# Performance work log

Hardware: AMD Instinct MI355X
Metric: run time of the kernel (lower is better)

Reference implementation:

```python
import jax, jax.numpy as jnp
import numpy as np

N_NODES = 100000
N_EDGES = 1600000
D = 128


def setup_inputs() -> dict:
    key = jax.random.key(0)
    ks = jax.random.split(key, 8)
    x = jax.random.normal(ks[0], (N_NODES, D), dtype=jnp.float32)
    edge_index = jax.random.randint(ks[1], (2, N_EDGES), 0, N_NODES, dtype=jnp.int64)
    # Linear weights ~ fan-in scaled init
    scale = 1.0 / np.sqrt(D)
    W1 = jax.random.normal(ks[2], (D, D), dtype=jnp.float32) * scale
    W2 = jax.random.normal(ks[3], (D, D), dtype=jnp.float32) * scale
    W3 = jax.random.normal(ks[4], (D, D), dtype=jnp.float32) * scale
    b1 = jnp.zeros((D,), jnp.float32)
    b2 = jnp.zeros((D,), jnp.float32)
    b3 = jnp.zeros((D,), jnp.float32)
    # train_eps=True, PyG initializes eps to 0
    eps1 = jnp.zeros((), jnp.float32)
    eps2 = jnp.zeros((), jnp.float32)
    eps3 = jnp.zeros((), jnp.float32)
    return {"x": x, "edge_index": edge_index,
            "W1": W1, "b1": b1, "eps1": eps1,
            "W2": W2, "b2": b2, "eps2": eps2,
            "W3": W3, "b3": b3, "eps3": eps3}


def _gin_conv(x, src, dst, eps, W, b):
    # scatter-add neighbor aggregation: sum_{j in N(i)} x_j
    agg = jax.ops.segment_sum(x[src], dst, num_segments=N_NODES)  # [N, D]
    h = (1.0 + eps) * x + agg
    return jax.nn.relu(h @ W + b)


def reference(x, edge_index, W1, b1, eps1, W2, b2, eps2, W3, b3, eps3):
    src, dst = edge_index[0], edge_index[1]
    h = _gin_conv(x, src, dst, eps1, W1, b1)   # conv1 (dropout p=0 -> identity)
    h = _gin_conv(h, src, dst, eps2, W2, b2)
    h = _gin_conv(h, src, dst, eps3, W3, b3)
    return jax.nn.log_softmax(h, axis=1)
```

## Files before the change

### kernel.cpp

```cpp
#include <hip/hip_runtime.h>
#include <hip/hip_bf16.h>

#define N_NODES 100000
#define N_EDGES 1600000
#define D 128
#define NRANGE 8
#define RANGE_SZ 12500
#define SB_PER_RANGE 196
#define NBUCKET (NRANGE * SB_PER_RANGE)
#define G_PART 512
#define CH_PART 3125
#define G_DEG 128
#define CH_DEG 784

typedef __attribute__((ext_vector_type(8))) short bf16x8;
typedef __attribute__((ext_vector_type(8))) unsigned short u16x8;
typedef __attribute__((ext_vector_type(4))) float f32x4;
typedef unsigned int u32;

__device__ inline ushort f2b(float x) {
    union { float f; unsigned u; } v; v.f = x;
    unsigned r = (v.u + 0x7fff + ((v.u >> 16) & 1)) >> 16;
    return (ushort)r;
}
__device__ inline float b2f(ushort b) {
    union { unsigned u; float f; } v; v.u = ((unsigned)b) << 16;
    return v.f;
}

__global__ void x2b_kernel(const float* __restrict__ x, ushort* __restrict__ xb) {
    int i = blockIdx.x * blockDim.x + threadIdx.x;
    if (i >= N_NODES * D / 4) return;
    float4 v = ((const float4*)x)[i];
    ushort4 o;
    o.x = f2b(v.x); o.y = f2b(v.y); o.z = f2b(v.z); o.w = f2b(v.w);
    ((ushort4*)xb)[i] = o;
}


__global__ void hist1_kernel(const int* __restrict__ dst, int* __restrict__ bhist1) {
    __shared__ int lh[NRANGE];
    if (threadIdx.x < NRANGE) lh[threadIdx.x] = 0;
    __syncthreads();
    int s0 = blockIdx.x * CH_PART, s1 = s0 + CH_PART;
    if (s1 > N_EDGES) s1 = N_EDGES;
    for (int i = s0 + threadIdx.x; i < s1; i += 256)
        atomicAdd(&lh[dst[i] / RANGE_SZ], 1);
    __syncthreads();
    if (threadIdx.x < NRANGE) bhist1[blockIdx.x * NRANGE + threadIdx.x] = lh[threadIdx.x];
}

__global__ void scan1_kernel(const int* __restrict__ bhist1, int* __restrict__ cbase1,
                             int* __restrict__ rs) {
    int r = threadIdx.x >> 6, lane = threadIdx.x & 63;
    __shared__ int rtot[NRANGE], roff[NRANGE];
    int excl[8];
    int run = 0;
    #pragma unroll
    for (int seg = 0; seg < 8; ++seg) {
        int b = seg * 64 + lane;
        int v = bhist1[b * NRANGE + r];
        int sc = v;
        #pragma unroll
        for (int off = 1; off < 64; off <<= 1) {
            int y = __shfl_up(sc, off);
            if (lane >= off) sc += y;
        }
        excl[seg] = run + sc - v;
        run += __shfl(sc, 63);
    }
    if (lane == 63) rtot[r] = run;
    __syncthreads();
    if (threadIdx.x == 0) {
        int a = 0;
        for (int i = 0; i < NRANGE; ++i) { roff[i] = a; a += rtot[i]; }
    }
    __syncthreads();
    int base = roff[r];
    #pragma unroll
    for (int seg = 0; seg < 8; ++seg)
        cbase1[(seg * 64 + lane) * NRANGE + r] = base + excl[seg];
    if (threadIdx.x < NRANGE) rs[threadIdx.x] = roff[threadIdx.x];
    if (threadIdx.x == 0) rs[NRANGE] = N_EDGES;
}

__global__ void place1_kernel(const int* __restrict__ src, const int* __restrict__ dst,
                              const int* __restrict__ cbase1, u32* __restrict__ epack1) {
    __shared__ int cur[NRANGE];
    if (threadIdx.x < NRANGE) cur[threadIdx.x] = cbase1[blockIdx.x * NRANGE + threadIdx.x];
    __syncthreads();
    int s0 = blockIdx.x * CH_PART, s1 = s0 + CH_PART;
    if (s1 > N_EDGES) s1 = N_EDGES;
    for (int i = s0 + threadIdx.x; i < s1; i += 256) {
        int d = dst[i], s = src[i];
        int r = d / RANGE_SZ;
        int dl = d - r * RANGE_SZ;
        int p = atomicAdd(&cur[r], 1);
        epack1[p] = ((u32)dl << 17) | (u32)s;
    }
}

__global__ void hist2_kernel(const u32* __restrict__ epack1, const int* __restrict__ rs,
                             int* __restrict__ bhist2) {
    __shared__ int lh[SB_PER_RANGE];
    for (int i = threadIdx.x; i < SB_PER_RANGE; i += 256) lh[i] = 0;
    __syncthreads();
    int r = blockIdx.x >> 6, j = blockIdx.x & 63;
    int e0 = rs[r], e1 = rs[r + 1];
    int cs = (e1 - e0 + 63) >> 6;
    int s0 = e0 + j * cs, s1 = s0 + cs;
    if (s1 > e1) s1 = e1;
    for (int i = s0 + threadIdx.x; i < s1; i += 256)
        atomicAdd(&lh[epack1[i] >> 23], 1);
    __syncthreads();
    for (int i = threadIdx.x; i < SB_PER_RANGE; i += 256)
        bhist2[blockIdx.x * SB_PER_RANGE + i] = lh[i];
}

__global__ void scan2_kernel(const int* __restrict__ bhist2, const int* __restrict__ rs,
                             int* __restrict__ cbase2, int* __restrict__ bucket_start) {
    int r = blockIdx.x;
    __shared__ int tot[SB_PER_RANGE];
    __shared__ int base[SB_PER_RANGE];
    int sb = threadIdx.x;
    if (sb < SB_PER_RANGE) {
        int s = 0;
        for (int j = 0; j < 64; ++j) s += bhist2[(r * 64 + j) * SB_PER_RANGE + sb];
        tot[sb] = s;
    }
    __syncthreads();
    if (threadIdx.x == 0) {
        int a = 0;
        for (int i = 0; i < SB_PER_RANGE; ++i) { base[i] = a; a += tot[i]; }
    }
    __syncthreads();
    if (sb < SB_PER_RANGE) {
        int run = rs[r] + base[sb];
        bucket_start[r * SB_PER_RANGE + sb] = run;
        for (int j = 0; j < 64; ++j) {
            cbase2[(r * 64 + j) * SB_PER_RANGE + sb] = run;
            run += bhist2[(r * 64 + j) * SB_PER_RANGE + sb];
        }
    }
    if (r == NRANGE - 1 && threadIdx.x == 0) bucket_start[NBUCKET] = N_EDGES;
}

__global__ void place2_kernel(const u32* __restrict__ epack1, const int* __restrict__ rs,
                              const int* __restrict__ cbase2, u32* __restrict__ epack2) {
    __shared__ int cur[SB_PER_RANGE];
    for (int i = threadIdx.x; i < SB_PER_RANGE; i += 256)
        cur[i] = cbase2[blockIdx.x * SB_PER_RANGE + i];
    __syncthreads();
    int r = blockIdx.x >> 6, j = blockIdx.x & 63;
    int e0 = rs[r], e1 = rs[r + 1];
    int cs = (e1 - e0 + 63) >> 6;
    int s0 = e0 + j * cs, s1 = s0 + cs;
    if (s1 > e1) s1 = e1;
    for (int i = s0 + threadIdx.x; i < s1; i += 256) {
        u32 e = epack1[i];
        int sb = e >> 23;
        int p = atomicAdd(&cur[sb], 1);
        epack2[p] = e & 0x7FFFFFu;
    }
}

__global__ void sort3_kernel(const u32* __restrict__ epack2, const int* __restrict__ bucket_start,
                             int* __restrict__ row_ptr, int* __restrict__ col,
                             int* __restrict__ deg) {
    int b = blockIdx.x;
    int r = b / SB_PER_RANGE, sb = b - r * SB_PER_RANGE;
    int node_base = r * RANGE_SZ + sb * 64;
    int nb = r * RANGE_SZ + RANGE_SZ - node_base;
    if (nb > 64) nb = 64;
    int e0 = bucket_start[b], e1 = bucket_start[b + 1];
    __shared__ int hist[64], cur[64];
    if (threadIdx.x < 64) hist[threadIdx.x] = 0;
    __syncthreads();
    for (int i = e0 + threadIdx.x; i < e1; i += 256)
        atomicAdd(&hist[(epack2[i] >> 17) & 63], 1);
    __syncthreads();
    if (threadIdx.x < 64) {
        int v = hist[threadIdx.x];
        int sc = v;
        #pragma unroll
        for (int off = 1; off < 64; off <<= 1) {
            int y = __shfl_up(sc, off);
            if (threadIdx.x >= off) sc += y;
        }
        int ex = e0 + sc - v;
        cur[threadIdx.x] = ex;
        if (threadIdx.x < nb) {
            row_ptr[node_base + threadIdx.x] = ex;
            deg[node_base + threadIdx.x] = v;
        }
    }
    __syncthreads();
    for (int i = e0 + threadIdx.x; i < e1; i += 256) {
        u32 e = epack2[i];
        int l = (e >> 17) & 63;
        int p = atomicAdd(&cur[l], 1);
        col[p] = (int)(e & 0x1FFFFu);
    }
    if (b == NBUCKET - 1 && threadIdx.x == 0) row_ptr[N_NODES] = N_EDGES;
}


__global__ void deghist_kernel(const int* __restrict__ deg, int* __restrict__ bdh) {
    __shared__ int lh[128];
    if (threadIdx.x < 128) lh[threadIdx.x] = 0;
    __syncthreads();
    int s0 = blockIdx.x * CH_DEG, s1 = s0 + CH_DEG;
    if (s1 > N_NODES) s1 = N_NODES;
    for (int i = s0 + threadIdx.x; i < s1; i += 256)
        atomicAdd(&lh[min(deg[i], 127)], 1);
    __syncthreads();
    if (threadIdx.x < 128) bdh[blockIdx.x * 128 + threadIdx.x] = lh[threadIdx.x];
}

__global__ void degscan_kernel(const int* __restrict__ bdh, int* __restrict__ cbdeg) {
    __shared__ int sh[128];
    int t = threadIdx.x;
    int tot = 0;
    for (int j = 0; j < G_DEG; ++j) tot += bdh[j * 128 + t];
    sh[t] = tot;
    __syncthreads();
    if (t == 0) {
        int run = 0;
        for (int b = 127; b >= 0; --b) { int c = sh[b]; sh[b] = run; run += c; }
    }
    __syncthreads();
    int run = sh[t];
    for (int j = 0; j < G_DEG; ++j) {
        cbdeg[j * 128 + t] = run;
        run += bdh[j * 128 + t];
    }
}

__global__ void degplace_kernel(const int* __restrict__ deg, const int* __restrict__ cbdeg,
                                int* __restrict__ perm) {
    __shared__ int cur[128];
    if (threadIdx.x < 128) cur[threadIdx.x] = cbdeg[blockIdx.x * 128 + threadIdx.x];
    __syncthreads();
    int s0 = blockIdx.x * CH_DEG, s1 = s0 + CH_DEG;
    if (s1 > N_NODES) s1 = N_NODES;
    for (int i = s0 + threadIdx.x; i < s1; i += 256) {
        int p = atomicAdd(&cur[min(deg[i], 127)], 1);
        perm[p] = i;
    }
}


__global__ void aggregate_kernel(const ushort* __restrict__ xb, const int* __restrict__ row_ptr,
                                 const int* __restrict__ col, const int* __restrict__ perm,
                                 const float* __restrict__ eps_p, ushort* __restrict__ hb) {
    int q = (blockIdx.x * blockDim.x + threadIdx.x) >> 4;
    if (q >= N_NODES) return;
    int node = perm[q];
    int l16 = threadIdx.x & 15;
    int beg = row_ptr[node], end = row_ptr[node + 1];
    float a0[8] = {0,0,0,0,0,0,0,0};
    float a1[8] = {0,0,0,0,0,0,0,0};
    int e = beg;
    for (; e + 7 < end; e += 8) {
        int s[8];
        #pragma unroll
        for (int j = 0; j < 8; ++j) s[j] = col[e + j];
        u16x8 v[8];
        #pragma unroll
        for (int j = 0; j < 8; ++j)
            v[j] = *(const u16x8*)(xb + ((size_t)s[j] << 7) + l16 * 8);
        #pragma unroll
        for (int j = 0; j < 8; ++j) {
            float* a = (j & 1) ? a1 : a0;
            #pragma unroll
            for (int k = 0; k < 8; ++k) a[k] += b2f(v[j][k]);
        }
    }
    if (e + 3 < end) {
        int s[4];
        #pragma unroll
        for (int j = 0; j < 4; ++j) s[j] = col[e + j];
        u16x8 v[4];
        #pragma unroll
        for (int j = 0; j < 4; ++j)
            v[j] = *(const u16x8*)(xb + ((size_t)s[j] << 7) + l16 * 8);
        #pragma unroll
        for (int j = 0; j < 4; ++j) {
            float* a = (j & 1) ? a1 : a0;
            #pragma unroll
            for (int k = 0; k < 8; ++k) a[k] += b2f(v[j][k]);
        }
        e += 4;
    }
    for (; e < end; ++e) {
        int s = col[e];
        u16x8 v = *(const u16x8*)(xb + ((size_t)s << 7) + l16 * 8);
        #pragma unroll
        for (int k = 0; k < 8; ++k) a0[k] += b2f(v[k]);
    }
    float scale = 1.0f + *eps_p;
    u16x8 xi = *(const u16x8*)(xb + ((size_t)node << 7) + l16 * 8);
    u16x8 ho;
    #pragma unroll
    for (int k = 0; k < 8; ++k) {
        float o = a0[k] + a1[k] + scale * b2f(xi[k]);
        ho[k] = f2b(o);
    }
    *(u16x8*)(hb + ((size_t)node << 7) + l16 * 8) = ho;
}

__global__ void wsplit3_kernel(const float* __restrict__ W1, const float* __restrict__ W2,
                               const float* __restrict__ W3,
                               ushort* __restrict__ wt_hi, ushort* __restrict__ wt_lo) {
    int layer = blockIdx.x >> 6;
    int t = (blockIdx.x & 63) * 256 + threadIdx.x;
    const float* W = layer == 0 ? W1 : layer == 1 ? W2 : W3;
    int k = t >> 7, n = t & 127;
    float w = W[t];
    ushort hi = f2b(w);
    ushort lo = f2b(w - b2f(hi));
    wt_hi[layer * D * D + n * D + k] = hi;
    wt_lo[layer * D * D + n * D + k] = lo;
}

template <int MODE>
__launch_bounds__(256, 2)
__global__ void gemm_relu_mfma(const ushort* __restrict__ hb,
                               const ushort* __restrict__ wt_hi, const ushort* __restrict__ wt_lo,
                               const float* __restrict__ bias,
                               float* __restrict__ outf, ushort* __restrict__ outb) {
    int wv = threadIdx.x >> 6, lane = threadIdx.x & 63;
    int r0 = blockIdx.x * 128 + wv * 32;
    int arow = lane & 15, agrp = lane >> 4;
    bf16x8 Ah[2][4];
    #pragma unroll
    for (int mf = 0; mf < 2; ++mf) {
        size_t rbase = (size_t)(r0 + mf * 16 + arow) * D;
        #pragma unroll
        for (int kf = 0; kf < 4; ++kf)
            Ah[mf][kf] = *(const bf16x8*)(hb + rbase + kf * 32 + agrp * 8);
    }
    f32x4 acc[2][8];
    #pragma unroll
    for (int mf = 0; mf < 2; ++mf)
        #pragma unroll
        for (int nf = 0; nf < 8; ++nf)
            acc[mf][nf] = (f32x4){0.f, 0.f, 0.f, 0.f};
    #pragma unroll
    for (int nf = 0; nf < 8; ++nf) {
        #pragma unroll
        for (int kf = 0; kf < 4; ++kf) {
            size_t wb = (size_t)(nf * 16 + arow) * D + kf * 32 + agrp * 8;
            bf16x8 bh = *(const bf16x8*)(wt_hi + wb);
            bf16x8 bl = *(const bf16x8*)(wt_lo + wb);
            #pragma unroll
            for (int mf = 0; mf < 2; ++mf) {
                acc[mf][nf] = __builtin_amdgcn_mfma_f32_16x16x32_bf16(Ah[mf][kf], bh, acc[mf][nf], 0, 0, 0);
                acc[mf][nf] = __builtin_amdgcn_mfma_f32_16x16x32_bf16(Ah[mf][kf], bl, acc[mf][nf], 0, 0, 0);
            }
        }
    }
    float bcol[8];
    #pragma unroll
    for (int nf = 0; nf < 8; ++nf) bcol[nf] = bias[nf * 16 + arow];
    if (MODE == 0) {
        int crow = agrp * 4;
        #pragma unroll
        for (int mf = 0; mf < 2; ++mf) {
            #pragma unroll
            for (int nf = 0; nf < 8; ++nf) {
                int coln = nf * 16 + arow;
                #pragma unroll
                for (int r = 0; r < 4; ++r) {
                    int row = r0 + mf * 16 + crow + r;
                    if (row < N_NODES)
                        outb[(size_t)row * D + coln] = f2b(fmaxf(acc[mf][nf][r] + bcol[nf], 0.f));
                }
            }
        }
    } else {
        #pragma unroll
        for (int mf = 0; mf < 2; ++mf) {
            #pragma unroll
            for (int rr = 0; rr < 4; ++rr) {
                float v[8];
                #pragma unroll
                for (int nf = 0; nf < 8; ++nf)
                    v[nf] = fmaxf(acc[mf][nf][rr] + bcol[nf], 0.f);
                float m = v[0];
                #pragma unroll
                for (int nf = 1; nf < 8; ++nf) m = fmaxf(m, v[nf]);
                #pragma unroll
                for (int off = 1; off < 16; off <<= 1) m = fmaxf(m, __shfl_xor(m, off));
                float s = 0.f;
                #pragma unroll
                for (int nf = 0; nf < 8; ++nf) s += __expf(v[nf] - m);
                #pragma unroll
                for (int off = 1; off < 16; off <<= 1) s += __shfl_xor(s, off);
                float lse = m + __logf(s);
                int row = r0 + mf * 16 + agrp * 4 + rr;
                if (row < N_NODES) {
                    #pragma unroll
                    for (int nf = 0; nf < 8; ++nf)
                        outf[(size_t)row * D + nf * 16 + arow] = v[nf] - lse;
                }
            }
        }
    }
}

extern "C" void kernel_launch(void* const* d_in, const int* in_sizes, int n_in,
                              void* d_out, int out_size, void* d_ws, size_t ws_size,
                              hipStream_t stream) {
    (void)in_sizes; (void)n_in; (void)out_size; (void)ws_size;
    const float* x  = (const float*)d_in[0];
    const int*   ei = (const int*)d_in[1];
    const int*   src = ei;
    const int*   dst = ei + N_EDGES;
    const float* W1 = (const float*)d_in[2];
    const float* b1 = (const float*)d_in[3];
    const float* e1 = (const float*)d_in[4];
    const float* W2 = (const float*)d_in[5];
    const float* b2 = (const float*)d_in[6];
    const float* e2 = (const float*)d_in[7];
    const float* W3 = (const float*)d_in[8];
    const float* b3 = (const float*)d_in[9];
    const float* e3 = (const float*)d_in[10];
    float* out = (float*)d_out;

    char* ws = (char*)d_ws;
    int*    rs           = (int*)ws;
    int*    bucket_start = (int*)(ws + 1024);
    int*    bhist1       = (int*)(ws + 8192);
    int*    cbase1       = (int*)(ws + 24576);
    int*    bhist2       = (int*)(ws + 40960);
    int*    cbase2       = (int*)(ws + 442368);
    int*    row_ptr      = (int*)(ws + 851968);
    int*    deg          = (int*)(ws + 1253376);
    int*    perm         = (int*)(ws + 1654784);
    int*    bdh          = (int*)(ws + 2055168);
    int*    cbdeg        = (int*)(ws + 2120704);
    int*    col          = (int*)(ws + 2193408);
    ushort* wt_hi        = (ushort*)(ws + 8650752);
    ushort* wt_lo        = (ushort*)(ws + 8749056);
    ushort* xb           = (ushort*)(ws + 9437184);
    ushort* hb           = (ushort*)(ws + 35651584);
    u32*    epack1       = (u32*)(ws + 35651584);
    u32*    epack2       = (u32*)(ws + 42991616);

    x2b_kernel<<<(N_NODES * D / 4 + 255) / 256, 256, 0, stream>>>(x, xb);

    hist1_kernel<<<G_PART, 256, 0, stream>>>(dst, bhist1);
    scan1_kernel<<<1, 512, 0, stream>>>(bhist1, cbase1, rs);
    place1_kernel<<<G_PART, 256, 0, stream>>>(src, dst, cbase1, epack1);
    hist2_kernel<<<G_PART, 256, 0, stream>>>(epack1, rs, bhist2);
    scan2_kernel<<<NRANGE, 256, 0, stream>>>(bhist2, rs, cbase2, bucket_start);
    place2_kernel<<<G_PART, 256, 0, stream>>>(epack1, rs, cbase2, epack2);
    sort3_kernel<<<NBUCKET, 256, 0, stream>>>(epack2, bucket_start, row_ptr, col, deg);

    deghist_kernel<<<G_DEG, 256, 0, stream>>>(deg, bdh);
    degscan_kernel<<<1, 128, 0, stream>>>(bdh, cbdeg);
    degplace_kernel<<<G_DEG, 256, 0, stream>>>(deg, cbdeg, perm);

    wsplit3_kernel<<<192, 256, 0, stream>>>(W1, W2, W3, wt_hi, wt_lo);

    const int aggGrid = (N_NODES * 16 + 255) / 256;
    const int gemmGrid = (N_NODES + 127) / 128;

    aggregate_kernel<<<aggGrid, 256, 0, stream>>>(xb, row_ptr, col, perm, e1, hb);
    gemm_relu_mfma<0><<<gemmGrid, 256, 0, stream>>>(hb, wt_hi, wt_lo, b1, nullptr, xb);
    aggregate_kernel<<<aggGrid, 256, 0, stream>>>(xb, row_ptr, col, perm, e2, hb);
    gemm_relu_mfma<0><<<gemmGrid, 256, 0, stream>>>(hb, wt_hi + D * D, wt_lo + D * D, b2, nullptr, xb);
    aggregate_kernel<<<aggGrid, 256, 0, stream>>>(hb  == nullptr ? hb : xb, row_ptr, col, perm, e3, hb);
    gemm_relu_mfma<1><<<gemmGrid, 256, 0, stream>>>(hb, wt_hi + 2 * D * D, wt_lo + 2 * D * D, b3, out, nullptr);
}
```

Baseline: 383.0 us.

## Fuse neighbor aggregation and MFMA GEMM into one per-layer kernel via LDS

Merges the aggregate kernel and the GEMM+ReLU kernel into a single per-layer kernel. Each block aggregates 64 degree-sorted nodes into shared memory, then runs the bf16 hi/lo MFMA GEMM on that tile and scatters the results to the original node rows through perm. This removes the global write and reload of the aggregated hidden tensor and one launch per layer, and ping-pongs between xb and hb. In exchange, every block reloads the full weight matrices for only 64 rows, output writes become scattered, and the aggregation and GEMM phases in a block no longer overlap across kernels.

```diff
diff --git a/kernel.cpp b/kernel.cpp
--- a/kernel.cpp
+++ b/kernel.cpp
@@ -247,66 +247,6 @@
         int p = atomicAdd(&cur[min(deg[i], 127)], 1);
         perm[p] = i;
     }
-}
-
-
-__global__ void aggregate_kernel(const ushort* __restrict__ xb, const int* __restrict__ row_ptr,
-                                 const int* __restrict__ col, const int* __restrict__ perm,
-                                 const float* __restrict__ eps_p, ushort* __restrict__ hb) {
-    int q = (blockIdx.x * blockDim.x + threadIdx.x) >> 4;
-    if (q >= N_NODES) return;
-    int node = perm[q];
-    int l16 = threadIdx.x & 15;
-    int beg = row_ptr[node], end = row_ptr[node + 1];
-    float a0[8] = {0,0,0,0,0,0,0,0};
-    float a1[8] = {0,0,0,0,0,0,0,0};
-    int e = beg;
-    for (; e + 7 < end; e += 8) {
-        int s[8];
-        #pragma unroll
-        for (int j = 0; j < 8; ++j) s[j] = col[e + j];
-        u16x8 v[8];
-        #pragma unroll
-        for (int j = 0; j < 8; ++j)
-            v[j] = *(const u16x8*)(xb + ((size_t)s[j] << 7) + l16 * 8);
-        #pragma unroll
-        for (int j = 0; j < 8; ++j) {
-            float* a = (j & 1) ? a1 : a0;
-            #pragma unroll
-            for (int k = 0; k < 8; ++k) a[k] += b2f(v[j][k]);
-        }
-    }
-    if (e + 3 < end) {
-        int s[4];
-        #pragma unroll
-        for (int j = 0; j < 4; ++j) s[j] = col[e + j];
-        u16x8 v[4];
-        #pragma unroll
-        for (int j = 0; j < 4; ++j)
-            v[j] = *(const u16x8*)(xb + ((size_t)s[j] << 7) + l16 * 8);
-        #pragma unroll
-        for (int j = 0; j < 4; ++j) {
-            float* a = (j & 1) ? a1 : a0;
-            #pragma unroll
-            for (int k = 0; k < 8; ++k) a[k] += b2f(v[j][k]);
-        }
-        e += 4;
-    }
-    for (; e < end; ++e) {
-        int s = col[e];
-        u16x8 v = *(const u16x8*)(xb + ((size_t)s << 7) + l16 * 8);
-        #pragma unroll
-        for (int k = 0; k < 8; ++k) a0[k] += b2f(v[k]);
-    }
-    float scale = 1.0f + *eps_p;
-    u16x8 xi = *(const u16x8*)(xb + ((size_t)node << 7) + l16 * 8);
-    u16x8 ho;
-    #pragma unroll
-    for (int k = 0; k < 8; ++k) {
-        float o = a0[k] + a1[k] + scale * b2f(xi[k]);
-        ho[k] = f2b(o);
-    }
-    *(u16x8*)(hb + ((size_t)node << 7) + l16 * 8) = ho;
 }
 
 __global__ void wsplit3_kernel(const float* __restrict__ W1, const float* __restrict__ W2,
@@ -323,29 +263,89 @@
     wt_lo[layer * D * D + n * D + k] = lo;
 }
 
+#define HL_STRIDE 136
 template <int MODE>
-__launch_bounds__(256, 2)
-__global__ void gemm_relu_mfma(const ushort* __restrict__ hb,
-                               const ushort* __restrict__ wt_hi, const ushort* __restrict__ wt_lo,
-                               const float* __restrict__ bias,
-                               float* __restrict__ outf, ushort* __restrict__ outb) {
-    int wv = threadIdx.x >> 6, lane = threadIdx.x & 63;
-    int r0 = blockIdx.x * 128 + wv * 32;
+__launch_bounds__(256, 4)
+__global__ void gin_layer_kernel(const ushort* __restrict__ xb, const int* __restrict__ row_ptr,
+                                 const int* __restrict__ col, const int* __restrict__ perm,
+                                 const float* __restrict__ eps_p,
+                                 const ushort* __restrict__ wt_hi, const ushort* __restrict__ wt_lo,
+                                 const float* __restrict__ bias,
+                                 float* __restrict__ outf, ushort* __restrict__ outb) {
+    __shared__ ushort hl[64 * HL_STRIDE];
+    __shared__ int nodebuf[64];
+    int t = threadIdx.x;
+    int qw = t >> 4, l16 = t & 15;
+    float scale = 1.0f + *eps_p;
+
+    #pragma unroll
+    for (int i = 0; i < 4; ++i) {
+        int li = qw * 4 + i;
+        int q = blockIdx.x * 64 + li;
+        int node = (q < N_NODES) ? perm[q] : -1;
+        if (l16 == 0) nodebuf[li] = node;
+        if (node >= 0) {
+            int beg = row_ptr[node], end = row_ptr[node + 1];
+            float a0[8] = {0,0,0,0,0,0,0,0};
+            float a1[8] = {0,0,0,0,0,0,0,0};
+            int e = beg;
+            for (; e + 7 < end; e += 8) {
+                int s[8];
+                #pragma unroll
+                for (int j = 0; j < 8; ++j) s[j] = col[e + j];
+                u16x8 v[8];
+                #pragma unroll
+                for (int j = 0; j < 8; ++j)
+                    v[j] = *(const u16x8*)(xb + ((size_t)s[j] << 7) + l16 * 8);
+                #pragma unroll
+                for (int j = 0; j < 8; ++j) {
+                    float* a = (j & 1) ? a1 : a0;
+                    #pragma unroll
+                    for (int k = 0; k < 8; ++k) a[k] += b2f(v[j][k]);
+                }
+            }
+            if (e + 3 < end) {
+                int s[4];
+                #pragma unroll
+                for (int j = 0; j < 4; ++j) s[j] = col[e + j];
+                u16x8 v[4];
+                #pragma unroll
+                for (int j = 0; j < 4; ++j)
+                    v[j] = *(const u16x8*)(xb + ((size_t)s[j] << 7) + l16 * 8);
+                #pragma unroll
+                for (int j = 0; j < 4; ++j) {
+                    float* a = (j & 1) ? a1 : a0;
+                    #pragma unroll
+                    for (int k = 0; k < 8; ++k) a[k] += b2f(v[j][k]);
+                }
+                e += 4;
+            }
+            for (; e < end; ++e) {
+                int s = col[e];
+                u16x8 v = *(const u16x8*)(xb + ((size_t)s << 7) + l16 * 8);
+                #pragma unroll
+                for (int k = 0; k < 8; ++k) a0[k] += b2f(v[k]);
+            }
+            u16x8 xi = *(const u16x8*)(xb + ((size_t)node << 7) + l16 * 8);
+            u16x8 ho;
+            #pragma unroll
+            for (int k = 0; k < 8; ++k)
+                ho[k] = f2b(a0[k] + a1[k] + scale * b2f(xi[k]));
+            *(u16x8*)(hl + li * HL_STRIDE + l16 * 8) = ho;
+        }
+    }
+    __syncthreads();
+
+    int wv = t >> 6, lane = t & 63;
     int arow = lane & 15, agrp = lane >> 4;
-    bf16x8 Ah[2][4];
-    #pragma unroll
-    for (int mf = 0; mf < 2; ++mf) {
-        size_t rbase = (size_t)(r0 + mf * 16 + arow) * D;
-        #pragma unroll
-        for (int kf = 0; kf < 4; ++kf)
-            Ah[mf][kf] = *(const bf16x8*)(hb + rbase + kf * 32 + agrp * 8);
-    }
-    f32x4 acc[2][8];
-    #pragma unroll
-    for (int mf = 0; mf < 2; ++mf)
-        #pragma unroll
-        for (int nf = 0; nf < 8; ++nf)
-            acc[mf][nf] = (f32x4){0.f, 0.f, 0.f, 0.f};
+    int lr0 = wv * 16;
+    bf16x8 Ah[4];
+    #pragma unroll
+    for (int kf = 0; kf < 4; ++kf)
+        Ah[kf] = *(const bf16x8*)(hl + (lr0 + arow) * HL_STRIDE + kf * 32 + agrp * 8);
+    f32x4 acc[8];
+    #pragma unroll
+    for (int nf = 0; nf < 8; ++nf) acc[nf] = (f32x4){0.f, 0.f, 0.f, 0.f};
     #pragma unroll
     for (int nf = 0; nf < 8; ++nf) {
         #pragma unroll
@@ -353,57 +353,47 @@
             size_t wb = (size_t)(nf * 16 + arow) * D + kf * 32 + agrp * 8;
             bf16x8 bh = *(const bf16x8*)(wt_hi + wb);
             bf16x8 bl = *(const bf16x8*)(wt_lo + wb);
-            #pragma unroll
-            for (int mf = 0; mf < 2; ++mf) {
-                acc[mf][nf] = __builtin_amdgcn_mfma_f32_16x16x32_bf16(Ah[mf][kf], bh, acc[mf][nf], 0, 0, 0);
-                acc[mf][nf] = __builtin_amdgcn_mfma_f32_16x16x32_bf16(Ah[mf][kf], bl, acc[mf][nf], 0, 0, 0);
-            }
+            acc[nf] = __builtin_amdgcn_mfma_f32_16x16x32_bf16(Ah[kf], bh, acc[nf], 0, 0, 0);
+            acc[nf] = __builtin_amdgcn_mfma_f32_16x16x32_bf16(Ah[kf], bl, acc[nf], 0, 0, 0);
         }
     }
     float bcol[8];
     #pragma unroll
     for (int nf = 0; nf < 8; ++nf) bcol[nf] = bias[nf * 16 + arow];
     if (MODE == 0) {
-        int crow = agrp * 4;
         #pragma unroll
-        for (int mf = 0; mf < 2; ++mf) {
-            #pragma unroll
-            for (int nf = 0; nf < 8; ++nf) {
-                int coln = nf * 16 + arow;
-                #pragma unroll
-                for (int r = 0; r < 4; ++r) {
-                    int row = r0 + mf * 16 + crow + r;
-                    if (row < N_NODES)
-                        outb[(size_t)row * D + coln] = f2b(fmaxf(acc[mf][nf][r] + bcol[nf], 0.f));
-                }
+        for (int nf = 0; nf < 8; ++nf) {
+            int coln = nf * 16 + arow;
+            #pragma unroll
+            for (int r = 0; r < 4; ++r) {
+                int node = nodebuf[lr0 + agrp * 4 + r];
+                if (node >= 0)
+                    outb[(size_t)node * D + coln] = f2b(fmaxf(acc[nf][r] + bcol[nf], 0.f));
             }
         }
     } else {
         #pragma unroll
-        for (int mf = 0; mf < 2; ++mf) {
-            #pragma unroll
-            for (int rr = 0; rr < 4; ++rr) {
-                float v[8];
+        for (int rr = 0; rr < 4; ++rr) {
+            int node = nodebuf[lr0 + agrp * 4 + rr];
+            float v[8];
+            #pragma unroll
+            for (int nf = 0; nf < 8; ++nf)
+                v[nf] = fmaxf(acc[nf][rr] + bcol[nf], 0.f);
+            float m = v[0];
+            #pragma unroll
+            for (int nf = 1; nf < 8; ++nf) m = fmaxf(m, v[nf]);
+            #pragma unroll
+            for (int off = 1; off < 16; off <<= 1) m = fmaxf(m, __shfl_xor(m, off));
+            float s = 0.f;
+            #pragma unroll
+            for (int nf = 0; nf < 8; ++nf) s += __expf(v[nf] - m);
+            #pragma unroll
+            for (int off = 1; off < 16; off <<= 1) s += __shfl_xor(s, off);
+            float lse = m + __logf(s);
+            if (node >= 0) {
                 #pragma unroll
                 for (int nf = 0; nf < 8; ++nf)
-                    v[nf] = fmaxf(acc[mf][nf][rr] + bcol[nf], 0.f);
-                float m = v[0];
-                #pragma unroll
-                for (int nf = 1; nf < 8; ++nf) m = fmaxf(m, v[nf]);
-                #pragma unroll
-                for (int off = 1; off < 16; off <<= 1) m = fmaxf(m, __shfl_xor(m, off));
-                float s = 0.f;
-                #pragma unroll
-                for (int nf = 0; nf < 8; ++nf) s += __expf(v[nf] - m);
-                #pragma unroll
-                for (int off = 1; off < 16; off <<= 1) s += __shfl_xor(s, off);
-                float lse = m + __logf(s);
-                int row = r0 + mf * 16 + agrp * 4 + rr;
-                if (row < N_NODES) {
-                    #pragma unroll
-                    for (int nf = 0; nf < 8; ++nf)
-                        outf[(size_t)row * D + nf * 16 + arow] = v[nf] - lse;
-                }
+                    outf[(size_t)node * D + nf * 16 + arow] = v[nf] - lse;
             }
         }
     }
@@ -464,13 +454,12 @@
 
     wsplit3_kernel<<<192, 256, 0, stream>>>(W1, W2, W3, wt_hi, wt_lo);
 
-    const int aggGrid = (N_NODES * 16 + 255) / 256;
-    const int gemmGrid = (N_NODES + 127) / 128;
-
-    aggregate_kernel<<<aggGrid, 256, 0, stream>>>(xb, row_ptr, col, perm, e1, hb);
-    gemm_relu_mfma<0><<<gemmGrid, 256, 0, stream>>>(hb, wt_hi, wt_lo, b1, nullptr, xb);
-    aggregate_kernel<<<aggGrid, 256, 0, stream>>>(xb, row_ptr, col, perm, e2, hb);
-    gemm_relu_mfma<0><<<gemmGrid, 256, 0, stream>>>(hb, wt_hi + D * D, wt_lo + D * D, b2, nullptr, xb);
-    aggregate_kernel<<<aggGrid, 256, 0, stream>>>(hb  == nullptr ? hb : xb, row_ptr, col, perm, e3, hb);
-    gemm_relu_mfma<1><<<gemmGrid, 256, 0, stream>>>(hb, wt_hi + 2 * D * D, wt_lo + 2 * D * D, b3, out, nullptr);
-}
+    const int layerGrid = (N_NODES + 63) / 64;
+
+    gin_layer_kernel<0><<<layerGrid, 256, 0, stream>>>(xb, row_ptr, col, perm, e1,
+                                                       wt_hi, wt_lo, b1, nullptr, hb);
+    gin_layer_kernel<0><<<layerGrid, 256, 0, stream>>>(hb, row_ptr, col, perm, e2,
+                                                       wt_hi + D * D, wt_lo + D * D, b2, nullptr, xb);
+    gin_layer_kernel<1><<<layerGrid, 256, 0, stream>>>(xb, row_ptr, col, perm, e3,
+                                                       wt_hi + 2 * D * D, wt_lo + 2 * D * D, b3, out, nullptr);
+}
```

After: 413.9 us. 1.08x slower.
